# Optimization experiments

Hardware: AMD Instinct MI355X
Metric: run time of the kernel (lower is better)

## Reference

```python
import jax, jax.numpy as jnp
import numpy as np

EMB_DIM = 1024
NUM_HEADS = 16
SCALE_WEIGHTS = 1.0
TINY = jnp.finfo(jnp.float32).tiny


def setup_inputs() -> dict:
    key = jax.random.key(0)
    k1, k2, k3 = jax.random.split(key, 3)
    B, S = 2, 2048
    x = jax.random.normal(k1, (B, S, EMB_DIM), dtype=jnp.float32)
    weights = jax.random.uniform(k2, (B, S), dtype=jnp.float32)
    W_qkv = jax.random.normal(k3, (EMB_DIM, 3 * EMB_DIM), dtype=jnp.float32) / np.sqrt(EMB_DIM)
    b_qkv = jnp.zeros((3 * EMB_DIM,), dtype=jnp.float32)
    return {"x": x, "weights": weights, "W_qkv": W_qkv, "b_qkv": b_qkv}


def reference(x, weights, W_qkv, b_qkv):
    B, S, E = x.shape
    H = NUM_HEADS
    hd = E // H
    # QKV projection: [B,S,3E] -> [B,H,S,3*hd] -> split
    qkv = x @ W_qkv + b_qkv
    qkv = qkv.reshape(B, S, H, 3 * hd).transpose(0, 2, 1, 3)
    q, k, v = jnp.split(qkv, 3, axis=-1)  # each [B,H,S,hd]
    # weights: [B,S] -> [B,1,1,S] (broadcast over heads and query positions)
    w = weights[:, None, None, :]
    # scores with log-weight bias and hard masks
    attn_logits = jnp.einsum("bhqd,bhkd->bhqk", q, k) / jnp.sqrt(jnp.asarray(hd, x.dtype))
    attn_logits = attn_logits + jnp.log(w / SCALE_WEIGHTS + TINY)
    attn_logits = jnp.where(w == 0, -9e15, attn_logits)
    attn_logits = jnp.where(w == 1, 9e15, attn_logits)
    attention = jax.nn.softmax(attn_logits, axis=-1)
    values = jnp.einsum("bhqk,bhkd->bhqd", attention, v)
    return values.transpose(0, 2, 1, 3).reshape(B, S, E)
```

## Files before the change

kernel.cpp:

```cpp
#include <hip/hip_runtime.h>
#include <math.h>

#define B_  2
#define S_  2048
#define E_  1024
#define H_  16
#define HD_ 64
#define N3_ 3072
#define M_  (B_*S_)

typedef _Float16 h8  __attribute__((ext_vector_type(8)));
typedef _Float16 h4  __attribute__((ext_vector_type(4)));
typedef float    f4  __attribute__((ext_vector_type(4)));
typedef float    fv16 __attribute__((ext_vector_type(16)));

typedef __attribute__((address_space(3))) unsigned int       lds_u32;
typedef const __attribute__((address_space(1))) unsigned int glob_u32;

__device__ __forceinline__ void gld16(const void* g, void* l) {
    __builtin_amdgcn_global_load_lds((glob_u32*)g, (lds_u32*)l, 16, 0, 0);
}
__device__ __forceinline__ float exp2_hw(float x) { return __builtin_amdgcn_exp2f(x); }

#define QSCALE 0.18033688011112042f

__global__ void cvt_x_kernel(const float* __restrict__ x, _Float16* __restrict__ x16) {
    int i = (blockIdx.x * 256 + threadIdx.x) * 8;
    float4 u = *(const float4*)&x[i];
    float4 v = *(const float4*)&x[i + 4];
    h8 o;
    o[0] = (_Float16)u.x; o[1] = (_Float16)u.y; o[2] = (_Float16)u.z; o[3] = (_Float16)u.w;
    o[4] = (_Float16)v.x; o[5] = (_Float16)v.y; o[6] = (_Float16)v.z; o[7] = (_Float16)v.w;
    *(h8*)&x16[i] = o;
}

__global__ __launch_bounds__(256) void transpose_w_kernel(
        const float* __restrict__ W, _Float16* __restrict__ Wt) {
    __shared__ float T[64][65];
    int k0 = blockIdx.x * 64, n0 = blockIdx.y * 64;
    int tid = threadIdx.x;
    int r = tid >> 4, c4 = (tid & 15) * 4;
#pragma unroll
    for (int i = 0; i < 4; i++) {
        int row = r + i * 16;
        float4 u = *(const float4*)&W[(size_t)(k0 + row) * N3_ + n0 + c4];
        T[c4 + 0][row] = u.x; T[c4 + 1][row] = u.y;
        T[c4 + 2][row] = u.z; T[c4 + 3][row] = u.w;
    }
    __syncthreads();
#pragma unroll
    for (int i = 0; i < 4; i++) {
        int rn = r + i * 16;
        h4 p;
        p[0] = (_Float16)T[rn][c4 + 0]; p[1] = (_Float16)T[rn][c4 + 1];
        p[2] = (_Float16)T[rn][c4 + 2]; p[3] = (_Float16)T[rn][c4 + 3];
        *(h4*)&Wt[(size_t)(n0 + rn) * E_ + k0 + c4] = p;
    }
}

__global__ __launch_bounds__(256, 2) void qkv_gemm32(
        const _Float16* __restrict__ x16, const _Float16* __restrict__ wt,
        const float* __restrict__ bq, const float* __restrict__ w,
        _Float16* __restrict__ qws, _Float16* __restrict__ kws,
        _Float16* __restrict__ vtws) {
    __shared__ __align__(16) _Float16 Ab[2][128 * 64];
    __shared__ __align__(16) _Float16 Wb[2][192 * 64];

    int tid = threadIdx.x;
    int wid = tid >> 6, lane = tid & 63;
    int l31 = lane & 31, hi = lane >> 5, l7 = l31 & 7;
    int srow = lane >> 3;
    int wm = wid & 1, wn = wid >> 1;

    int L = blockIdx.x;
    int head = 2 * (L & 7) + (L >> 8);
    int mb = (L >> 3) & 31;
    int m0 = mb * 128;
    int n0 = head * 192;
    int b = m0 >> 11;
    int bh = b * H_ + head;
    int sblk = m0 & 2047;

    fv16 acc[2][3];
#pragma unroll
    for (int ntl = 0; ntl < 3; ntl++) {
        int n_abs = wn * 96 + ntl * 32;
        int which = n_abs >> 6;
        fv16 ini;
        if (which == 2) {
            float bb = bq[n0 + n_abs + l31];
#pragma unroll
            for (int r = 0; r < 16; r++) ini[r] = bb;
        } else {
#pragma unroll
            for (int g = 0; g < 4; g++) {
                f4 bv = *(const f4*)&bq[n0 + n_abs + 8 * g + 4 * hi];
#pragma unroll
                for (int j = 0; j < 4; j++) ini[4 * g + j] = bv[j];
            }
        }
        acc[0][ntl] = ini; acc[1][ntl] = ini;
    }

    auto stage = [&](int t, int bf) {
        int k0 = t * 64;
#pragma unroll
        for (int j = 0; j < 4; j++) {
            int batch = wid * 4 + j;
            int row = batch * 8 + srow;
            int ch = (lane & 7) ^ srow ^ (batch & 7);
            gld16(&x16[(size_t)(m0 + row) * E_ + k0 + ch * 8], &Ab[bf][batch * 8 * 64]);
        }
#pragma unroll
        for (int j = 0; j < 6; j++) {
            int batch = wid * 6 + j;
            int row = batch * 8 + srow;
            int ch = (lane & 7) ^ srow ^ (batch & 7);
            gld16(&wt[(size_t)(n0 + row) * E_ + k0 + ch * 8], &Wb[bf][batch * 8 * 64]);
        }
    };

    stage(0, 0);

    for (int t = 0; t < 16; t++) {
        int bf = t & 1;
        __syncthreads();
        if (t < 15) stage(t + 1, bf ^ 1);
#pragma unroll
        for (int step = 0; step < 4; step++) {
            h8 af[2], wf[3];
#pragma unroll
            for (int mt = 0; mt < 2; mt++) {
                int R = wm * 64 + mt * 32 + l31;
                int ph = ((2 * step + hi) ^ l7 ^ ((mt * 4 + (l31 >> 3)) & 7)) * 8;
                af[mt] = *(const h8*)&Ab[bf][R * 64 + ph];
            }
#pragma unroll
            for (int ntl = 0; ntl < 3; ntl++) {
                int R = wn * 96 + ntl * 32 + l31;
                int ph = ((2 * step + hi) ^ l7 ^ ((wn * 12 + ntl * 4 + (l31 >> 3)) & 7)) * 8;
                wf[ntl] = *(const h8*)&Wb[bf][R * 64 + ph];
            }
#pragma unroll
            for (int ntl = 0; ntl < 3; ntl++) {
                bool isv = (wn == 1) && (ntl >= 1);
#pragma unroll
                for (int mt = 0; mt < 2; mt++) {
                    if (isv)
                        acc[mt][ntl] = __builtin_amdgcn_mfma_f32_32x32x16_f16(af[mt], wf[ntl], acc[mt][ntl], 0, 0, 0);
                    else
                        acc[mt][ntl] = __builtin_amdgcn_mfma_f32_32x32x16_f16(wf[ntl], af[mt], acc[mt][ntl], 0, 0, 0);
                }
            }
        }
    }

#pragma unroll
    for (int ntl = 0; ntl < 3; ntl++) {
        int n_abs = wn * 96 + ntl * 32;
        int which = n_abs >> 6;
#pragma unroll
        for (int mt = 0; mt < 2; mt++) {
            if (which == 2) {
                int d = (n_abs & 63) + l31;
#pragma unroll
                for (int g = 0; g < 4; g++) {
                    int soff = wm * 64 + mt * 32 + 8 * g + 4 * hi;
                    f4 wf4 = *(const f4*)&w[m0 + soff];
                    h4 p;
#pragma unroll
                    for (int j = 0; j < 4; j++)
                        p[j] = (_Float16)(acc[mt][ntl][4 * g + j] * wf4[j]);
                    *(h4*)&vtws[((size_t)bh * 64 + d) * S_ + sblk + soff] = p;
                }
            } else {
                _Float16* dst = (which == 0) ? qws : kws;
                float scale = (which == 0) ? QSCALE : 1.0f;
                int s = sblk + wm * 64 + mt * 32 + l31;
#pragma unroll
                for (int g = 0; g < 4; g++) {
                    int d0 = (n_abs & 63) + 8 * g + 4 * hi;
                    h4 p;
#pragma unroll
                    for (int j = 0; j < 4; j++)
                        p[j] = (_Float16)(acc[mt][ntl][4 * g + j] * scale);
                    *(h4*)&dst[((size_t)bh * S_ + s) * 64 + d0] = p;
                }
            }
        }
    }
}

__global__ __launch_bounds__(256, 2) void attn_kernel(
        const _Float16* __restrict__ q, const _Float16* __restrict__ k,
        const _Float16* __restrict__ vt, const float* __restrict__ w,
        float* __restrict__ out) {
    __shared__ __align__(16) _Float16 Kb[2][64 * 64];
    __shared__ __align__(16) _Float16 Vb[2][64 * 64];
    __shared__ __align__(16) float lws[2048];

    int tid = threadIdx.x;
    int wid = tid >> 6, lane = tid & 63;
    int l31 = lane & 31, hi = lane >> 5, l7 = l31 & 7;
    int srow = lane >> 3;
    int L = blockIdx.x;
    int bh = (L & 7) + 8 * (L >> 7);
    int qt = (L >> 3) & 15;
    int q0 = qt * 128;
    int b = bh >> 4, h = bh & 15;

    const _Float16* qbase = q + (size_t)bh * S_ * HD_;
    const _Float16* kbase = k + (size_t)bh * S_ * HD_;
    const _Float16* vbase = vt + (size_t)bh * HD_ * S_;
    const float* wbase = w + (size_t)b * S_;

#pragma unroll
    for (int j = 0; j < 2; j++) {
        int batch = wid + 4 * j;
        gld16(&wbase[batch * 256 + lane * 4], &lws[batch * 256]);
    }

    auto stage = [&](int kt, int bf) {
        int k0 = kt * 64;
#pragma unroll
        for (int j = 0; j < 2; j++) {
            int batch = wid * 2 + j;
            int row = batch * 8 + srow;
            int ch = (lane & 7) ^ srow ^ (batch & 7);
            gld16(&kbase[(size_t)(k0 + row) * 64 + ch * 8], &Kb[bf][batch * 8 * 64]);
            gld16(&vbase[(size_t)row * S_ + k0 + ch * 8], &Vb[bf][batch * 8 * 64]);
        }
    };

    stage(0, 0);

    int qrow = q0 + wid * 32 + l31;
    h8 qf[4];
#pragma unroll
    for (int step = 0; step < 4; step++)
        qf[step] = *(const h8*)&qbase[(size_t)qrow * 64 + 16 * step + 8 * hi];

    fv16 o[2];
    o[0] = (fv16)0.0f; o[1] = (fv16)0.0f;
    float m_r = -INFINITY, l_r = 0.0f;

    for (int kt = 0; kt < 32; kt++) {
        int bf = kt & 1;
        __syncthreads();
        if (kt < 31) stage(kt + 1, bf ^ 1);

        fv16 st[2];
        st[0] = (fv16)0.0f; st[1] = (fv16)0.0f;
#pragma unroll
        for (int step = 0; step < 4; step++) {
#pragma unroll
            for (int kt2 = 0; kt2 < 2; kt2++) {
                int R = kt2 * 32 + l31;
                int ph = ((2 * step + hi) ^ l7 ^ ((kt2 * 4 + (l31 >> 3)) & 7)) * 8;
                h8 kf = *(const h8*)&Kb[bf][R * 64 + ph];
                st[kt2] = __builtin_amdgcn_mfma_f32_32x32x16_f16(kf, qf[step], st[kt2], 0, 0, 0);
            }
        }

        float rm = -INFINITY;
#pragma unroll
        for (int kt2 = 0; kt2 < 2; kt2++)
#pragma unroll
            for (int r = 0; r < 16; r++) rm = fmaxf(rm, st[kt2][r]);
        rm = fmaxf(rm, __shfl_xor(rm, 32));
        float mnew = fmaxf(m_r, rm);
        float rs = 0.0f;
        h4 pf[2][4];
        int k0 = kt * 64;
#pragma unroll
        for (int kt2 = 0; kt2 < 2; kt2++)
#pragma unroll
            for (int g = 0; g < 4; g++) {
                f4 wv = *(const f4*)&lws[k0 + kt2 * 32 + 8 * g + 4 * hi];
                f4 e;
#pragma unroll
                for (int j = 0; j < 4; j++) {
                    float ev = exp2_hw(st[kt2][4 * g + j] - mnew);
                    e[j] = ev;
                    rs += ev * wv[j];
                }
                h4 p;
                p[0] = (_Float16)e[0]; p[1] = (_Float16)e[1];
                p[2] = (_Float16)e[2]; p[3] = (_Float16)e[3];
                pf[kt2][g] = p;
            }
        rs += __shfl_xor(rs, 32);
        float alpha = exp2_hw(m_r - mnew);
        m_r = mnew;
        l_r = l_r * alpha + rs;
        o[0] = o[0] * alpha;
        o[1] = o[1] * alpha;

#pragma unroll
        for (int kt2 = 0; kt2 < 2; kt2++)
#pragma unroll
            for (int g = 0; g < 4; g++) {
                int c = 4 * kt2 + g;
#pragma unroll
                for (int dt = 0; dt < 2; dt++) {
                    int R = dt * 32 + l31;
                    int ph = (c ^ l7 ^ ((dt * 4 + (l31 >> 3)) & 7)) * 8 + hi * 4;
                    h4 vf = *(const h4*)&Vb[bf][R * 64 + ph];
                    o[dt] = __builtin_amdgcn_mfma_f32_32x32x8f16(vf, pf[kt2][g], o[dt], 0, 0, 0);
                }
            }
    }

    float linv = 1.0f / l_r;
    float* obase = &out[((size_t)(b * S_ + qrow)) * E_ + h * 64];
#pragma unroll
    for (int dt = 0; dt < 2; dt++)
#pragma unroll
        for (int g = 0; g < 4; g++) {
            int d0 = dt * 32 + 8 * g + 4 * hi;
            f4 ov;
#pragma unroll
            for (int j = 0; j < 4; j++) ov[j] = o[dt][4 * g + j] * linv;
            *(f4*)&obase[d0] = ov;
        }
}

extern "C" void kernel_launch(void* const* d_in, const int* in_sizes, int n_in,
                              void* d_out, int out_size, void* d_ws, size_t ws_size,
                              hipStream_t stream) {
    const float* x  = (const float*)d_in[0];
    const float* w  = (const float*)d_in[1];
    const float* Wq = (const float*)d_in[2];
    const float* bq = (const float*)d_in[3];
    float* out = (float*)d_out;

    char* p = (char*)d_ws;
    _Float16* x16 = (_Float16*)p;              p += (size_t)M_ * E_ * 2;
    _Float16* wt  = (_Float16*)p;              p += (size_t)E_ * N3_ * 2;
    _Float16* qb  = (_Float16*)p;              p += (size_t)M_ * E_ * 2;
    _Float16* kb  = (_Float16*)p;              p += (size_t)M_ * E_ * 2;
    _Float16* vtb = (_Float16*)p;

    cvt_x_kernel<<<dim3(M_ * E_ / 2048), dim3(256), 0, stream>>>(x, x16);
    transpose_w_kernel<<<dim3(E_ / 64, N3_ / 64), dim3(256), 0, stream>>>(Wq, wt);
    qkv_gemm32<<<dim3(512), dim3(256), 0, stream>>>(x16, wt, bq, w, qb, kb, vtb);
    attn_kernel<<<dim3(512), dim3(256), 0, stream>>>(qb, kb, vtb, w, out);
}
```

Baseline: 181.5 us.

## Split attention KV range across two wave groups with LDS merge

Doubles the attention block to 512 threads. Two groups of four waves each process half of the key/value sequence for the same 128 query rows, then merge their partial softmax states (max, sum, output) through LDS before writing. Staging is reorganized so half the waves load K and half load V. The per-block weights LDS buffer is dropped in favour of direct global loads. This raises wave-level parallelism and halves the serial KV loop, at the cost of a merge step, more LDS per block, and possible register pressure under the tighter launch bounds.

```diff
diff --git a/kernel.cpp b/kernel.cpp
--- a/kernel.cpp
+++ b/kernel.cpp
@@ -191,18 +191,19 @@
     }
 }
 
-__global__ __launch_bounds__(256, 2) void attn_kernel(
+__global__ __launch_bounds__(512, 4) void attn_kernel(
         const _Float16* __restrict__ q, const _Float16* __restrict__ k,
         const _Float16* __restrict__ vt, const float* __restrict__ w,
         float* __restrict__ out) {
-    __shared__ __align__(16) _Float16 Kb[2][64 * 64];
-    __shared__ __align__(16) _Float16 Vb[2][64 * 64];
-    __shared__ __align__(16) float lws[2048];
+    __shared__ __align__(16) _Float16 Kb[2][2][64 * 64];
+    __shared__ __align__(16) _Float16 Vb[2][2][64 * 64];
 
     int tid = threadIdx.x;
     int wid = tid >> 6, lane = tid & 63;
     int l31 = lane & 31, hi = lane >> 5, l7 = l31 & 7;
     int srow = lane >> 3;
+    int s = wid >> 2;
+    int w4 = wid & 3;
     int L = blockIdx.x;
     int bh = (L & 7) + 8 * (L >> 7);
     int qt = (L >> 3) & 15;
@@ -214,27 +215,26 @@
     const _Float16* vbase = vt + (size_t)bh * HD_ * S_;
     const float* wbase = w + (size_t)b * S_;
 
-#pragma unroll
-    for (int j = 0; j < 2; j++) {
-        int batch = wid + 4 * j;
-        gld16(&wbase[batch * 256 + lane * 4], &lws[batch * 256]);
-    }
-
-    auto stage = [&](int kt, int bf) {
-        int k0 = kt * 64;
-#pragma unroll
-        for (int j = 0; j < 2; j++) {
-            int batch = wid * 2 + j;
-            int row = batch * 8 + srow;
-            int ch = (lane & 7) ^ srow ^ (batch & 7);
-            gld16(&kbase[(size_t)(k0 + row) * 64 + ch * 8], &Kb[bf][batch * 8 * 64]);
-            gld16(&vbase[(size_t)row * S_ + k0 + ch * 8], &Vb[bf][batch * 8 * 64]);
+    int skv = (wid >> 1) & 1;
+    int bt0 = (wid & 1) * 4;
+
+    auto stage = [&](int t, int bf) {
+        int k0 = (s * 16 + t) * 64;
+#pragma unroll
+        for (int j = 0; j < 4; j++) {
+            int bt = bt0 + j;
+            int row = bt * 8 + srow;
+            int ch = l7 ^ srow ^ bt;
+            if (skv == 0)
+                gld16(&kbase[(size_t)(k0 + row) * 64 + ch * 8], &Kb[s][bf][bt * 8 * 64]);
+            else
+                gld16(&vbase[(size_t)row * S_ + k0 + ch * 8], &Vb[s][bf][bt * 8 * 64]);
         }
     };
 
     stage(0, 0);
 
-    int qrow = q0 + wid * 32 + l31;
+    int qrow = q0 + w4 * 32 + l31;
     h8 qf[4];
 #pragma unroll
     for (int step = 0; step < 4; step++)
@@ -244,10 +244,10 @@
     o[0] = (fv16)0.0f; o[1] = (fv16)0.0f;
     float m_r = -INFINITY, l_r = 0.0f;
 
-    for (int kt = 0; kt < 32; kt++) {
-        int bf = kt & 1;
+    for (int t = 0; t < 16; t++) {
+        int bf = t & 1;
         __syncthreads();
-        if (kt < 31) stage(kt + 1, bf ^ 1);
+        if (t < 15) stage(t + 1, bf ^ 1);
 
         fv16 st[2];
         st[0] = (fv16)0.0f; st[1] = (fv16)0.0f;
@@ -257,11 +257,12 @@
             for (int kt2 = 0; kt2 < 2; kt2++) {
                 int R = kt2 * 32 + l31;
                 int ph = ((2 * step + hi) ^ l7 ^ ((kt2 * 4 + (l31 >> 3)) & 7)) * 8;
-                h8 kf = *(const h8*)&Kb[bf][R * 64 + ph];
+                h8 kf = *(const h8*)&Kb[s][bf][R * 64 + ph];
                 st[kt2] = __builtin_amdgcn_mfma_f32_32x32x16_f16(kf, qf[step], st[kt2], 0, 0, 0);
             }
         }
 
+        int k0 = (s * 16 + t) * 64;
         float rm = -INFINITY;
 #pragma unroll
         for (int kt2 = 0; kt2 < 2; kt2++)
@@ -271,12 +272,11 @@
         float mnew = fmaxf(m_r, rm);
         float rs = 0.0f;
         h4 pf[2][4];
-        int k0 = kt * 64;
 #pragma unroll
         for (int kt2 = 0; kt2 < 2; kt2++)
 #pragma unroll
             for (int g = 0; g < 4; g++) {
-                f4 wv = *(const f4*)&lws[k0 + kt2 * 32 + 8 * g + 4 * hi];
+                f4 wv = *(const f4*)&wbase[k0 + kt2 * 32 + 8 * g + 4 * hi];
                 f4 e;
 #pragma unroll
                 for (int j = 0; j < 4; j++) {
@@ -305,24 +305,50 @@
                 for (int dt = 0; dt < 2; dt++) {
                     int R = dt * 32 + l31;
                     int ph = (c ^ l7 ^ ((dt * 4 + (l31 >> 3)) & 7)) * 8 + hi * 4;
-                    h4 vf = *(const h4*)&Vb[bf][R * 64 + ph];
+                    h4 vf = *(const h4*)&Vb[s][bf][R * 64 + ph];
                     o[dt] = __builtin_amdgcn_mfma_f32_32x32x8f16(vf, pf[kt2][g], o[dt], 0, 0, 0);
                 }
             }
     }
 
-    float linv = 1.0f / l_r;
-    float* obase = &out[((size_t)(b * S_ + qrow)) * E_ + h * 64];
-#pragma unroll
-    for (int dt = 0; dt < 2; dt++)
-#pragma unroll
-        for (int g = 0; g < 4; g++) {
-            int d0 = dt * 32 + 8 * g + 4 * hi;
-            f4 ov;
-#pragma unroll
-            for (int j = 0; j < 4; j++) ov[j] = o[dt][4 * g + j] * linv;
-            *(f4*)&obase[d0] = ov;
-        }
+    float* mO = (float*)&Kb[0][0][0];
+    float* mML = (float*)&Vb[0][0][0];
+    int qloc = w4 * 32 + l31;
+
+    __syncthreads();
+    if (s == 1) {
+#pragma unroll
+        for (int dt = 0; dt < 2; dt++)
+#pragma unroll
+            for (int r = 0; r < 16; r++) {
+                int d = dt * 32 + (r & 3) + 8 * (r >> 2) + 4 * hi;
+                mO[d * 128 + qloc] = o[dt][r];
+            }
+        if (hi == 0) {
+            mML[qloc * 2] = m_r;
+            mML[qloc * 2 + 1] = l_r;
+        }
+    }
+    __syncthreads();
+    if (s == 0) {
+        float m2 = mML[qloc * 2], l2 = mML[qloc * 2 + 1];
+        float mm = fmaxf(m_r, m2);
+        float a0 = exp2_hw(m_r - mm), a1 = exp2_hw(m2 - mm);
+        float linv = 1.0f / (l_r * a0 + l2 * a1);
+        a0 *= linv; a1 *= linv;
+        float* obase = &out[((size_t)(b * S_ + q0 + qloc)) * E_ + h * 64];
+#pragma unroll
+        for (int dt = 0; dt < 2; dt++)
+#pragma unroll
+            for (int g = 0; g < 4; g++) {
+                int d0 = dt * 32 + 8 * g + 4 * hi;
+                f4 ov;
+#pragma unroll
+                for (int j = 0; j < 4; j++)
+                    ov[j] = o[dt][4 * g + j] * a0 + mO[(d0 + j) * 128 + qloc] * a1;
+                *(f4*)&obase[d0] = ov;
+            }
+    }
 }
 
 extern "C" void kernel_launch(void* const* d_in, const int* in_sizes, int n_in,
@@ -344,5 +370,5 @@
     cvt_x_kernel<<<dim3(M_ * E_ / 2048), dim3(256), 0, stream>>>(x, x16);
     transpose_w_kernel<<<dim3(E_ / 64, N3_ / 64), dim3(256), 0, stream>>>(Wq, wt);
     qkv_gemm32<<<dim3(512), dim3(256), 0, stream>>>(x16, wt, bq, w, qb, kb, vtb);
-    attn_kernel<<<dim3(512), dim3(256), 0, stream>>>(qb, kb, vtb, w, out);
-}
+    attn_kernel<<<dim3(512), dim3(512), 0, stream>>>(qb, kb, vtb, w, out);
+}
```

Result: slower. 191.1 us (+5.3%).
